# Kernel optimization log

Hardware: AMD Instinct MI355X
Metric: run time of the kernel (lower is better)

## Reference

```python
import jax, jax.numpy as jnp
import numpy as np

K = 32          # num_cones
D = 512         # decoder feature dim (feature_mapper in_features)
VOX = 32 * 32 * 32
N = 524288      # query points
EPS = 1e-8

CONE_ADDER = jnp.array([-0.8, -0.8, -0.8, 0.05, 0.1, -1.0, -1.0, -1.0], jnp.float32)
CONE_MULT = jnp.array([1.0, 1.0, 1.0, 0.01, 0.03, 1.7, 1.7, 1.7], jnp.float32)


def setup_inputs() -> dict:
    key = jax.random.key(0)
    ks = jax.random.split(key, 8)
    return {
        "voxel_data": jax.random.normal(ks[0], (1, VOX), jnp.float32),
        "query_points": jax.random.uniform(ks[1], (N, 3), jnp.float32, minval=-1.0, maxval=1.0),
        "initial_centers": jax.random.normal(ks[2], (K, 3), jnp.float32) * 0.3,
        # learned params (encoder MLP -> 512, decoder MLP 512->512, feature_mapper 512->K*8)
        "W_enc": jax.random.normal(ks[3], (VOX, D), jnp.float32) * 0.01,
        "b_enc": jnp.zeros((D,), jnp.float32),
        "W_dec": jax.random.normal(ks[4], (D, D), jnp.float32) * 0.04,
        "b_dec": jnp.zeros((D,), jnp.float32),
        "W_map": jax.random.normal(ks[5], (D, K * 8), jnp.float32) * 0.04,
        "b_map": jnp.zeros((K * 8,), jnp.float32),
    }


def determine_cone_sdf(q, p):
    # q: [N,3] query points; p: [K,8] = center(3), radius, height, orientation(3)
    centers = p[:, 0:3]            # [K,3]
    radii = p[:, 3]                # [K]
    heights = p[:, 4]              # [K]
    orient = p[:, 5:8]             # [K,3]
    axis = orient / (jnp.linalg.norm(orient, axis=-1, keepdims=True) + EPS)  # [K,3]
    v = q[:, None, :] - centers[None, :, :]                # [N,K,3]
    proj = jnp.einsum("nkd,kd->nk", v, axis)               # signed dist along axis [N,K]
    perp = jnp.linalg.norm(v - proj[..., None] * axis[None, :, :], axis=-1)  # [N,K]
    # lateral (slanted) surface: radius tapers linearly from base (proj=0) to apex (proj=height)
    slant = perp - radii[None, :] * (1.0 - proj / (heights[None, :] + EPS))
    cap = jnp.abs(proj) - heights[None, :]                 # end caps
    return jnp.maximum(slant, cap)                         # [N,K]


def reference(voxel_data, query_points, initial_centers,
              W_enc, b_enc, W_dec, b_dec, W_map, b_map):
    # encoder (global feature) -> decoder -> feature_mapper
    feat = jax.nn.relu(voxel_data @ W_enc + b_enc)     # [1, D]
    dec = jax.nn.relu(feat @ W_dec + b_dec)            # [1, D]
    cone_params = (dec @ W_map + b_map).reshape(K, 8)  # [K, 8]
    # sigmoid + affine rescale into valid geometric ranges
    cone_params = jax.nn.sigmoid(cone_params) * CONE_MULT + CONE_ADDER
    cone_sdf = determine_cone_sdf(query_points, cone_params)  # [N, K]
    return cone_sdf, cone_params
```

## Files before the change

kernel.cpp:

```cpp
#include <hip/hip_runtime.h>
#include <math.h>

#define VOX 32768
#define DD 512
#define KC 32
#define NQ 524288
#define EPSF 1e-8f
#define CONE_STRIDE 13

__device__ __constant__ float c_mult[8]  = {1.f, 1.f, 1.f, 0.01f, 0.03f, 1.7f, 1.7f, 1.7f};
__device__ __constant__ float c_adder[8] = {-0.8f, -0.8f, -0.8f, 0.05f, 0.1f, -1.f, -1.f, -1.f};

__global__ __launch_bounds__(512) void k_enc(const float* __restrict__ vox,
                                             const float* __restrict__ Wenc,
                                             float* __restrict__ dst,
                                             float* __restrict__ zbase,
                                             int mode) {
    __shared__ float4 red4[512];
    const int t = threadIdx.x;
    const int b = blockIdx.x;
    if (b == 0) {
        zbase[t] = 0.f;
        if (t < 256) zbase[512 + t] = 0.f;
    }
    const int g  = t >> 7;
    const int c4 = (t & 127) << 2;
    const int v0 = b * 64;
    float4 acc = make_float4(0.f, 0.f, 0.f, 0.f);
    #pragma unroll
    for (int it = 0; it < 16; ++it) {
        const int v = v0 + it * 4 + g;
        const float sv = vox[v];
        const float4 w = *reinterpret_cast<const float4*>(&Wenc[(size_t)v * DD + c4]);
        acc.x += sv * w.x; acc.y += sv * w.y; acc.z += sv * w.z; acc.w += sv * w.w;
    }
    red4[t] = acc;
    __syncthreads();
    const float* red = reinterpret_cast<const float*>(red4);
    const float s = red[t] + red[512 + t] + red[1024 + t] + red[1536 + t];
    if (mode) dst[(size_t)t * 512 + b] = s;
    else      atomicAdd(&dst[t], s);
}

__global__ __launch_bounds__(512) void k_dec(const float* __restrict__ src,
                                             const float* __restrict__ benc,
                                             const float* __restrict__ Wdec,
                                             float* __restrict__ decsum,
                                             int mode) {
    __shared__ float4 red4[512];
    __shared__ float wsum[8];
    const int t = threadIdx.x;
    const int g = t >> 7;
    const int j = t & 127;
    const int i = blockIdx.x * 4 + g;
    float f;
    if (mode) {
        const float4 pv = *reinterpret_cast<const float4*>(&src[(size_t)i * 512 + j * 4]);
        float s = pv.x + pv.y + pv.z + pv.w;
        #pragma unroll
        for (int off = 32; off >= 1; off >>= 1) s += __shfl_xor(s, off, 64);
        if ((t & 63) == 0) wsum[t >> 6] = s;
        __syncthreads();
        f = wsum[2 * g] + wsum[2 * g + 1];
    } else {
        f = src[i];
    }
    float fi = f + benc[i];
    fi = fi > 0.f ? fi : 0.f;
    const int c4 = j << 2;
    const float4 w = *reinterpret_cast<const float4*>(&Wdec[(size_t)i * DD + c4]);
    red4[t] = make_float4(fi * w.x, fi * w.y, fi * w.z, fi * w.w);
    __syncthreads();
    const float* red = reinterpret_cast<const float*>(red4);
    const float s2 = red[t] + red[512 + t] + red[1024 + t] + red[1536 + t];
    atomicAdd(&decsum[t], s2);
}

__global__ __launch_bounds__(256) void k_map(const float* __restrict__ decsum,
                                             const float* __restrict__ bdec,
                                             const float* __restrict__ Wmap,
                                             float* __restrict__ mapsum) {
    const int j  = threadIdx.x;
    const int i0 = blockIdx.x * 8;
    float acc = 0.f;
    #pragma unroll
    for (int r = 0; r < 8; ++r) {
        const int i = i0 + r;
        float di = decsum[i] + bdec[i];
        di = di > 0.f ? di : 0.f;
        acc += di * Wmap[(size_t)i * 256 + j];
    }
    atomicAdd(&mapsum[j], acc);
}

__global__ __launch_bounds__(256) void k_params(const float* __restrict__ mapsum,
                                                const float* __restrict__ bmap,
                                                float* __restrict__ out_params,
                                                float* __restrict__ cones) {
    __shared__ float p[256];
    const int j = threadIdx.x;
    const float s = mapsum[j] + bmap[j];
    const float sig = 1.f / (1.f + expf(-s));
    const float val = sig * c_mult[j & 7] + c_adder[j & 7];
    out_params[j] = val;
    p[j] = val;
    __syncthreads();
    if (j < KC) {
        const float cx = p[j*8+0], cy = p[j*8+1], cz = p[j*8+2];
        const float r  = p[j*8+3], h  = p[j*8+4];
        const float ox = p[j*8+5], oy = p[j*8+6], oz = p[j*8+7];
        const float nrm = sqrtf(ox*ox + oy*oy + oz*oz) + EPSF;
        const float inv = 1.f / nrm;
        const float inv_h = 1.f / (h + EPSF);
        float* ck = &cones[j * CONE_STRIDE];
        ck[0] = cx;      ck[1] = cy;      ck[2] = cz;
        ck[3] = ox*inv;  ck[4] = oy*inv;  ck[5] = oz*inv;
        ck[6] = r;       ck[7] = h;       ck[8] = inv_h;
        ck[9] = r * inv_h; ck[10] = 0.f;  ck[11] = 0.f;  ck[12] = 0.f;
    }
}

__global__ __launch_bounds__(256) void k_sdf(const float* __restrict__ q,
                                             const float* __restrict__ cones,
                                             float* __restrict__ out) {
    __shared__ float sq[96];
    __shared__ float c[KC * CONE_STRIDE];
    const int t = threadIdx.x;
    const size_t n0 = (size_t)blockIdx.x * 32;
    if (t < 96) sq[t] = q[n0 * 3 + t];
    c[t] = cones[t];
    if (t < KC * CONE_STRIDE - 256) c[256 + t] = cones[256 + t];
    __syncthreads();
    const int nl = t >> 3;
    const int k0 = (t & 7) << 2;
    const float qx = sq[nl*3+0], qy = sq[nl*3+1], qz = sq[nl*3+2];
    float4 o;
    float* of = &o.x;
    #pragma unroll
    for (int kk = 0; kk < 4; ++kk) {
        const float* ck = &c[(k0 + kk) * CONE_STRIDE];
        const float vx = qx - ck[0];
        const float vy = qy - ck[1];
        const float vz = qz - ck[2];
        const float proj = vx*ck[3] + vy*ck[4] + vz*ck[5];
        const float d2 = vx*vx + vy*vy + vz*vz;
        float pp = d2 - proj * proj;
        pp = pp > 0.f ? pp : 0.f;
        const float perp = sqrtf(pp);
        const float slant = perp - ck[6] + ck[9] * proj;
        const float cap = fabsf(proj) - ck[7];
        of[kk] = slant > cap ? slant : cap;
    }
    *reinterpret_cast<float4*>(&out[(n0 + nl) * (size_t)KC + k0]) = o;
}

extern "C" void kernel_launch(void* const* d_in, const int* in_sizes, int n_in,
                              void* d_out, int out_size, void* d_ws, size_t ws_size,
                              hipStream_t stream) {
    const float* vox  = (const float*)d_in[0];
    const float* q    = (const float*)d_in[1];
    const float* Wenc = (const float*)d_in[3];
    const float* benc = (const float*)d_in[4];
    const float* Wdec = (const float*)d_in[5];
    const float* bdec = (const float*)d_in[6];
    const float* Wmap = (const float*)d_in[7];
    const float* bmap = (const float*)d_in[8];
    float* out = (float*)d_out;
    float* ws  = (float*)d_ws;

    const size_t PART_FLOATS = 512 * 512;
    const size_t need = (PART_FLOATS + 512 + 256 + KC * CONE_STRIDE) * sizeof(float);
    const int mode = (ws_size >= need) ? 1 : 0;

    float *dst, *decsum, *mapsum, *cones;
    if (mode) {
        dst    = ws;
        decsum = ws + PART_FLOATS;
        mapsum = decsum + 512;
        cones  = mapsum + 256;
    } else {
        dst    = ws;
        decsum = ws + 512;
        mapsum = ws + 1024;
        cones  = ws + 1280;
        hipMemsetAsync(dst, 0, 512 * sizeof(float), stream);
    }

    k_enc<<<512, 512, 0, stream>>>(vox, Wenc, dst, decsum, mode);
    k_dec<<<128, 512, 0, stream>>>(dst, benc, Wdec, decsum, mode);
    k_map<<<64, 256, 0, stream>>>(decsum, bdec, Wmap, mapsum);
    k_params<<<1, 256, 0, stream>>>(mapsum, bmap, out + (size_t)NQ * KC, cones);
    k_sdf<<<NQ / 32, 256, 0, stream>>>(q, cones, out);
}
```

Baseline: 49.40 us.

## Replace atomics with partial buffers and fuse params into map via last-block reduction

The encoder, decoder and mapper stages now write deterministic partial sums instead of using atomicAdd. The separate params kernel is folded into the map kernel through a last-block-done counter. Scratch buffers live in the output tensor, which the SDF kernel overwrites afterwards, so only the counter and cone table stay in the workspace and the workspace-size fallback path is gone. This saves one launch and the atomic contention, at the cost of a threadfence and counter handshake plus a serial final reduction in one block.

```diff
diff --git a/kernel.cpp b/kernel.cpp
--- a/kernel.cpp
+++ b/kernel.cpp
@@ -1,28 +1,27 @@
 #include <hip/hip_runtime.h>
 #include <math.h>
 
-#define VOX 32768
 #define DD 512
 #define KC 32
 #define NQ 524288
 #define EPSF 1e-8f
 #define CONE_STRIDE 13
 
+#define OFF_PART 0
+#define OFF_DECP 262144
+#define OFF_MAPP 327680
+
 __device__ __constant__ float c_mult[8]  = {1.f, 1.f, 1.f, 0.01f, 0.03f, 1.7f, 1.7f, 1.7f};
 __device__ __constant__ float c_adder[8] = {-0.8f, -0.8f, -0.8f, 0.05f, 0.1f, -1.f, -1.f, -1.f};
 
 __global__ __launch_bounds__(512) void k_enc(const float* __restrict__ vox,
                                              const float* __restrict__ Wenc,
-                                             float* __restrict__ dst,
-                                             float* __restrict__ zbase,
-                                             int mode) {
+                                             float* __restrict__ partialT,
+                                             unsigned int* __restrict__ cnt) {
     __shared__ float4 red4[512];
     const int t = threadIdx.x;
     const int b = blockIdx.x;
-    if (b == 0) {
-        zbase[t] = 0.f;
-        if (t < 256) zbase[512 + t] = 0.f;
-    }
+    if (b == 0 && t == 0) *cnt = 0u;
     const int g  = t >> 7;
     const int c4 = (t & 127) << 2;
     const int v0 = b * 64;
@@ -38,85 +37,100 @@
     __syncthreads();
     const float* red = reinterpret_cast<const float*>(red4);
     const float s = red[t] + red[512 + t] + red[1024 + t] + red[1536 + t];
-    if (mode) dst[(size_t)t * 512 + b] = s;
-    else      atomicAdd(&dst[t], s);
+    partialT[(size_t)t * 512 + b] = s;
 }
 
-__global__ __launch_bounds__(512) void k_dec(const float* __restrict__ src,
+__global__ __launch_bounds__(512) void k_dec(const float* __restrict__ partialT,
                                              const float* __restrict__ benc,
                                              const float* __restrict__ Wdec,
-                                             float* __restrict__ decsum,
-                                             int mode) {
+                                             float* __restrict__ decPart) {
     __shared__ float4 red4[512];
     __shared__ float wsum[8];
     const int t = threadIdx.x;
     const int g = t >> 7;
     const int j = t & 127;
     const int i = blockIdx.x * 4 + g;
-    float f;
-    if (mode) {
-        const float4 pv = *reinterpret_cast<const float4*>(&src[(size_t)i * 512 + j * 4]);
-        float s = pv.x + pv.y + pv.z + pv.w;
-        #pragma unroll
-        for (int off = 32; off >= 1; off >>= 1) s += __shfl_xor(s, off, 64);
-        if ((t & 63) == 0) wsum[t >> 6] = s;
-        __syncthreads();
-        f = wsum[2 * g] + wsum[2 * g + 1];
-    } else {
-        f = src[i];
-    }
-    float fi = f + benc[i];
+    const float4 pv = *reinterpret_cast<const float4*>(&partialT[(size_t)i * 512 + j * 4]);
+    float s = pv.x + pv.y + pv.z + pv.w;
+    #pragma unroll
+    for (int off = 32; off >= 1; off >>= 1) s += __shfl_xor(s, off, 64);
+    if ((t & 63) == 0) wsum[t >> 6] = s;
+    __syncthreads();
+    float fi = wsum[2 * g] + wsum[2 * g + 1] + benc[i];
     fi = fi > 0.f ? fi : 0.f;
-    const int c4 = j << 2;
-    const float4 w = *reinterpret_cast<const float4*>(&Wdec[(size_t)i * DD + c4]);
+    const float4 w = *reinterpret_cast<const float4*>(&Wdec[(size_t)i * DD + (j << 2)]);
     red4[t] = make_float4(fi * w.x, fi * w.y, fi * w.z, fi * w.w);
     __syncthreads();
     const float* red = reinterpret_cast<const float*>(red4);
     const float s2 = red[t] + red[512 + t] + red[1024 + t] + red[1536 + t];
-    atomicAdd(&decsum[t], s2);
+    decPart[(size_t)blockIdx.x * 512 + t] = s2;
 }
 
-__global__ __launch_bounds__(256) void k_map(const float* __restrict__ decsum,
+__global__ __launch_bounds__(512) void k_map(const float* __restrict__ decPart,
                                              const float* __restrict__ bdec,
                                              const float* __restrict__ Wmap,
-                                             float* __restrict__ mapsum) {
-    const int j  = threadIdx.x;
-    const int i0 = blockIdx.x * 8;
+                                             float* __restrict__ mapPart,
+                                             const float* __restrict__ bmap,
+                                             float* __restrict__ out_params,
+                                             float* __restrict__ cones,
+                                             unsigned int* __restrict__ cnt) {
+    __shared__ float dec8[8];
+    __shared__ float half0[256];
+    __shared__ float pbuf[256];
+    __shared__ int lastflag;
+    const int t = threadIdx.x;
+    const int b = blockIdx.x;
+    const int w = t >> 6, l = t & 63;
+    const int i = b * 8 + w;
+    float s = decPart[(size_t)(2 * l) * 512 + i] + decPart[(size_t)(2 * l + 1) * 512 + i];
+    #pragma unroll
+    for (int off = 32; off >= 1; off >>= 1) s += __shfl_xor(s, off, 64);
+    if (l == 0) {
+        const float d = s + bdec[i];
+        dec8[w] = d > 0.f ? d : 0.f;
+    }
+    __syncthreads();
+    const int j = t & 255, h = t >> 8;
     float acc = 0.f;
     #pragma unroll
-    for (int r = 0; r < 8; ++r) {
-        const int i = i0 + r;
-        float di = decsum[i] + bdec[i];
-        di = di > 0.f ? di : 0.f;
-        acc += di * Wmap[(size_t)i * 256 + j];
+    for (int r = 0; r < 4; ++r) {
+        const int row = h * 4 + r;
+        acc += dec8[row] * Wmap[(size_t)(b * 8 + row) * 256 + j];
     }
-    atomicAdd(&mapsum[j], acc);
-}
-
-__global__ __launch_bounds__(256) void k_params(const float* __restrict__ mapsum,
-                                                const float* __restrict__ bmap,
-                                                float* __restrict__ out_params,
-                                                float* __restrict__ cones) {
-    __shared__ float p[256];
-    const int j = threadIdx.x;
-    const float s = mapsum[j] + bmap[j];
-    const float sig = 1.f / (1.f + expf(-s));
-    const float val = sig * c_mult[j & 7] + c_adder[j & 7];
-    out_params[j] = val;
-    p[j] = val;
+    if (h == 0) half0[j] = acc;
     __syncthreads();
-    if (j < KC) {
-        const float cx = p[j*8+0], cy = p[j*8+1], cz = p[j*8+2];
-        const float r  = p[j*8+3], h  = p[j*8+4];
-        const float ox = p[j*8+5], oy = p[j*8+6], oz = p[j*8+7];
+    if (h == 1) mapPart[(size_t)b * 256 + j] = half0[j] + acc;
+    __threadfence();
+    __syncthreads();
+    if (t == 0) lastflag = (atomicAdd(cnt, 1u) == 63u) ? 1 : 0;
+    __syncthreads();
+    if (!lastflag) return;
+    __threadfence();
+    float m = 0.f;
+    #pragma unroll 8
+    for (int p = h * 32; p < h * 32 + 32; ++p) m += mapPart[(size_t)p * 256 + j];
+    if (h == 0) half0[j] = m;
+    __syncthreads();
+    if (h == 1) {
+        const float tot = half0[j] + m + bmap[j];
+        const float sig = 1.f / (1.f + expf(-tot));
+        const float val = sig * c_mult[j & 7] + c_adder[j & 7];
+        out_params[j] = val;
+        pbuf[j] = val;
+    }
+    __syncthreads();
+    if (t < KC) {
+        const float cx = pbuf[t*8+0], cy = pbuf[t*8+1], cz = pbuf[t*8+2];
+        const float r  = pbuf[t*8+3], hh = pbuf[t*8+4];
+        const float ox = pbuf[t*8+5], oy = pbuf[t*8+6], oz = pbuf[t*8+7];
         const float nrm = sqrtf(ox*ox + oy*oy + oz*oz) + EPSF;
         const float inv = 1.f / nrm;
-        const float inv_h = 1.f / (h + EPSF);
-        float* ck = &cones[j * CONE_STRIDE];
-        ck[0] = cx;      ck[1] = cy;      ck[2] = cz;
-        ck[3] = ox*inv;  ck[4] = oy*inv;  ck[5] = oz*inv;
-        ck[6] = r;       ck[7] = h;       ck[8] = inv_h;
-        ck[9] = r * inv_h; ck[10] = 0.f;  ck[11] = 0.f;  ck[12] = 0.f;
+        const float inv_h = 1.f / (hh + EPSF);
+        float* ck = &cones[t * CONE_STRIDE];
+        ck[0] = cx;       ck[1] = cy;      ck[2] = cz;
+        ck[3] = ox * inv; ck[4] = oy * inv; ck[5] = oz * inv;
+        ck[6] = r;        ck[7] = hh;      ck[8] = inv_h;
+        ck[9] = r * inv_h; ck[10] = 0.f;   ck[11] = 0.f;  ck[12] = 0.f;
     }
 }
 
@@ -168,27 +182,17 @@
     float* out = (float*)d_out;
     float* ws  = (float*)d_ws;
 
-    const size_t PART_FLOATS = 512 * 512;
-    const size_t need = (PART_FLOATS + 512 + 256 + KC * CONE_STRIDE) * sizeof(float);
-    const int mode = (ws_size >= need) ? 1 : 0;
+    unsigned int* cnt = (unsigned int*)ws;
+    float* cones      = ws + 16;
 
-    float *dst, *decsum, *mapsum, *cones;
-    if (mode) {
-        dst    = ws;
-        decsum = ws + PART_FLOATS;
-        mapsum = decsum + 512;
-        cones  = mapsum + 256;
-    } else {
-        dst    = ws;
-        decsum = ws + 512;
-        mapsum = ws + 1024;
-        cones  = ws + 1280;
-        hipMemsetAsync(dst, 0, 512 * sizeof(float), stream);
-    }
+    float* partialT = out + OFF_PART;
+    float* decPart  = out + OFF_DECP;
+    float* mapPart  = out + OFF_MAPP;
+    float* out_params = out + (size_t)NQ * KC;
 
-    k_enc<<<512, 512, 0, stream>>>(vox, Wenc, dst, decsum, mode);
-    k_dec<<<128, 512, 0, stream>>>(dst, benc, Wdec, decsum, mode);
-    k_map<<<64, 256, 0, stream>>>(decsum, bdec, Wmap, mapsum);
-    k_params<<<1, 256, 0, stream>>>(mapsum, bmap, out + (size_t)NQ * KC, cones);
+    k_enc<<<512, 512, 0, stream>>>(vox, Wenc, partialT, cnt);
+    k_dec<<<128, 512, 0, stream>>>(partialT, benc, Wdec, decPart);
+    k_map<<<64, 512, 0, stream>>>(decPart, bdec, Wmap, mapPart,
+                                  bmap, out_params, cones, cnt);
     k_sdf<<<NQ / 32, 256, 0, stream>>>(q, cones, out);
 }
```

Measured after the change: 56.05 us. 13.5% more time.
